# Optimization experiments

Measured on AMD Instinct MI355X. Metric: run time of the kernel, lower is better.

Reference implementation:

```python
import jax, jax.numpy as jnp
import numpy as np

DELTA_VAR = 0.5
DELTA_DIST = 1.5
ALPHA = 1.0
BETA = 1.0
GAMMA = 0.001
IGNORE = 0
C = 20  # static label count: max(target)+1 with labels drawn from [0, 20)


def setup_inputs() -> dict:
    key = jax.random.key(0)
    k1, k2 = jax.random.split(key)
    emb = jax.random.normal(k1, (4, 16, 400, 800), dtype=jnp.float32)
    target = jax.random.randint(k2, (4, 400, 800), 0, 20, dtype=jnp.int32)
    return {"emb": emb, "target": target}


def _safe_norm(sq):
    # L2 norm from squared distance with zero-safe sqrt (matches torch.norm fwd,
    # and gives finite grads at 0 like torch's subgradient convention)
    nz = sq > 0
    return jnp.sqrt(jnp.where(nz, sq, 1.0)) * nz.astype(sq.dtype)


def _loss_one(x, lab):
    # x: (E, H, W), lab: (H, W) int labels in [0, C)
    E = x.shape[0]
    xf = x.reshape(E, -1).T          # (P, E)
    lf = lab.reshape(-1)             # (P,)
    dt = xf.dtype

    counts = jax.ops.segment_sum(jnp.ones_like(lf, dtype=dt), lf, num_segments=C)  # (C,)
    sums = jax.ops.segment_sum(xf, lf, num_segments=C)                              # (C, E)
    means = sums / counts[:, None]                                                  # (C, E)

    keep = jnp.array([c for c in range(C) if c != IGNORE])  # static
    Ck = C - 1
    means_k = means[keep]            # (Ck, E)
    counts_k = counts[keep]          # (Ck,)

    # --- variance (pull) term: distance of each pixel to its own cluster mean ---
    mean_px = means[lf]                                   # (P, E) gather
    d = _safe_norm(jnp.sum((xf - mean_px) ** 2, axis=1))  # (P,)
    mask = (lf != IGNORE).astype(dt)
    hinge = mask * jnp.maximum(d - DELTA_VAR, 0.0) ** 2
    var_per_inst = jax.ops.segment_sum(hinge, lf, num_segments=C)[keep] / counts_k
    variance_term = jnp.sum(var_per_inst) / Ck

    # --- distance (push) term: pairwise hinge between kept cluster means ---
    diff = means_k[:, None, :] - means_k[None, :, :]      # (Ck, Ck, E)
    dm = _safe_norm(jnp.sum(diff ** 2, axis=-1))          # (Ck, Ck)
    repulsion = 2.0 * DELTA_DIST * (1.0 - jnp.eye(Ck, dtype=dt))
    hinged = jnp.maximum(repulsion - dm, 0.0) ** 2
    distance_term = jnp.sum(hinged) / (Ck * (Ck - 1))

    # --- regularizer: mean norm of cluster means ---
    reg_term = jnp.sum(_safe_norm(jnp.sum(means_k ** 2, axis=1))) / Ck

    return ALPHA * variance_term + BETA * distance_term + GAMMA * reg_term


def reference(emb, target):
    losses = jax.vmap(_loss_one)(emb, target)  # (N,)
    return (jnp.sum(losses) / emb.shape[0])[None]  # shape (1,) like torch
```

## Files before the change

kernel.cpp:

```cpp
#include <hip/hip_runtime.h>

#define N_IMG 4
#define E_DIM 16
#define G_PIX 80000
#define C_CLS 20
#define CK 19
#define NREP 8
#define EG 4
#define NEG (E_DIM / EG)
#define SL1 64
#define R1 (G_PIX / SL1)
#define GRID1 (SL1 * NEG * N_IMG)
#define SL2 256
#define R2 ((G_PIX + SL2 - 1) / SL2)
#define GRID2 (SL2 * N_IMG)
#define MSTRIDE 17
#define LS_SLOT 5
#define SCALE_F 16777216.0f
#define INV_SCALE (1.0f / 16777216.0f)

#define SUMS_OFF 0
#define CNT_OFF (N_IMG * C_CLS * E_DIM)
#define LOSS_OFF (CNT_OFF + N_IMG * C_CLS)
#define WS_FLOATS (LOSS_OFF + 1)

static_assert(G_PIX % SL1 == 0, "k_sums slicing must be exact");

__global__ __launch_bounds__(256, 4) void k_sums(const float* __restrict__ emb,
                                                 const int* __restrict__ target,
                                                 float* __restrict__ ws) {
    __shared__ unsigned long long ls[C_CLS][NREP][LS_SLOT];
    __shared__ unsigned int lc[C_CLS][NREP];

    const int tid = threadIdx.x;
    const int b = blockIdx.x;
    const int n = b & 3;
    const int eg = (b >> 2) & (NEG - 1);
    const int slice = b >> 4;
    const int e0 = eg * EG;

    unsigned long long* lsf = &ls[0][0][0];
    for (int i = tid; i < C_CLS * NREP * LS_SLOT; i += 256) lsf[i] = 0ull;
    for (int i = tid; i < C_CLS * NREP; i += 256) (&lc[0][0])[i] = 0u;
    __syncthreads();

    const float4* emb0 = (const float4*)emb + ((size_t)(n * E_DIM + e0)) * G_PIX;
    const int4* tgt4 = (const int4*)target + (size_t)n * G_PIX;
    const int r = tid & (NREP - 1);

#define QADD(p, idx, val) \
    atomicAdd((p) + (idx), (unsigned long long)(long long)__float2int_rn((val) * SCALE_F))

    const int g1 = (slice + 1) * R1;
    for (int g = slice * R1 + tid; g < g1; g += 256) {
        const int4 lb = tgt4[g];
        const float4 v0 = emb0[g];
        const float4 v1 = emb0[G_PIX + g];
        const float4 v2 = emb0[2 * G_PIX + g];
        const float4 v3 = emb0[3 * G_PIX + g];

        unsigned long long* px = &ls[lb.x][r][0];
        unsigned long long* py = &ls[lb.y][r][0];
        unsigned long long* pz = &ls[lb.z][r][0];
        unsigned long long* pw = &ls[lb.w][r][0];
        QADD(px, 0, v0.x); QADD(px, 1, v1.x); QADD(px, 2, v2.x); QADD(px, 3, v3.x);
        QADD(py, 0, v0.y); QADD(py, 1, v1.y); QADD(py, 2, v2.y); QADD(py, 3, v3.y);
        QADD(pz, 0, v0.z); QADD(pz, 1, v1.z); QADD(pz, 2, v2.z); QADD(pz, 3, v3.z);
        QADD(pw, 0, v0.w); QADD(pw, 1, v1.w); QADD(pw, 2, v2.w); QADD(pw, 3, v3.w);
        if (eg == 0) {
            atomicAdd(&lc[lb.x][r], 1u); atomicAdd(&lc[lb.y][r], 1u);
            atomicAdd(&lc[lb.z][r], 1u); atomicAdd(&lc[lb.w][r], 1u);
        }
    }
#undef QADD
    __syncthreads();

    for (int i = tid; i < C_CLS * EG; i += 256) {
        const int c = i >> 2, e1 = i & 3;
        long long q = 0;
#pragma unroll
        for (int rr = 0; rr < NREP; rr++) q += (long long)ls[c][rr][e1];
        atomicAdd(ws + SUMS_OFF + (n * C_CLS + c) * E_DIM + e0 + e1, (float)q * INV_SCALE);
    }
    if (eg == 0) {
        for (int c = tid; c < C_CLS; c += 256) {
            unsigned int s = 0;
#pragma unroll
            for (int rr = 0; rr < NREP; rr++) s += lc[c][rr];
            atomicAdd(ws + CNT_OFF + n * C_CLS + c, (float)s);
        }
    }
}

__global__ __launch_bounds__(256, 4) void k_var(const float* __restrict__ emb,
                                                const int* __restrict__ target,
                                                float* __restrict__ ws) {
    __shared__ float lmean[C_CLS * MSTRIDE];
    __shared__ float lw[C_CLS];
    __shared__ float red[256];

    const int tid = threadIdx.x;
    const int b = blockIdx.x;
    const int n = b & 3;
    const int s2 = b >> 2;

    const float* gsum = ws + SUMS_OFF + n * C_CLS * E_DIM;
    const float* gcnt = ws + CNT_OFF + n * C_CLS;

    for (int i = tid; i < C_CLS * E_DIM; i += 256) {
        const int c = i >> 4, e = i & 15;
        const float cnt = gcnt[c];
        lmean[c * MSTRIDE + e] = (cnt > 0.f) ? gsum[i] / cnt : 0.f;
    }
    if (tid < C_CLS) {
        const float cnt = gcnt[tid];
        lw[tid] = (tid != 0 && cnt > 0.f) ? 1.0f / (cnt * (float)CK) : 0.f;
    }
    __syncthreads();

    float acc = 0.f;
    if (b < N_IMG) {
        for (int idx = tid; idx < CK * CK; idx += 256) {
            const int i = idx / CK + 1, j = idx % CK + 1;
            if (i != j) {
                float sq = 0.f;
#pragma unroll
                for (int e = 0; e < E_DIM; e++) {
                    const float d = lmean[i * MSTRIDE + e] - lmean[j * MSTRIDE + e];
                    sq += d * d;
                }
                const float dm = sqrtf(sq);
                const float h = fmaxf(3.0f - dm, 0.f);
                acc += h * h;
            }
        }
        acc *= 1.0f / (float)(CK * (CK - 1));
        float racc = 0.f;
        for (int c = tid + 1; c < C_CLS; c += 256) {
            float sq = 0.f;
#pragma unroll
            for (int e = 0; e < E_DIM; e++) {
                const float m = lmean[c * MSTRIDE + e];
                sq += m * m;
            }
            racc += sqrtf(sq);
        }
        acc += 0.001f * racc / (float)CK;
    }

    const float4* emb4 = (const float4*)emb + (size_t)n * E_DIM * G_PIX;
    const int4* tgt4 = (const int4*)target + (size_t)n * G_PIX;
    const int gend0 = (s2 + 1) * R2;
    const int gend = (gend0 < G_PIX) ? gend0 : G_PIX;
    for (int g = s2 * R2 + tid; g < gend; g += 256) {
        const int4 lb = tgt4[g];
        const int bx = lb.x * MSTRIDE, by = lb.y * MSTRIDE;
        const int bz = lb.z * MSTRIDE, bw = lb.w * MSTRIDE;
        float sx = 0.f, sy = 0.f, sz = 0.f, sw = 0.f;
#pragma unroll
        for (int e = 0; e < E_DIM; e++) {
            const float4 v = emb4[(size_t)e * G_PIX + g];
            float d;
            d = v.x - lmean[bx + e]; sx += d * d;
            d = v.y - lmean[by + e]; sy += d * d;
            d = v.z - lmean[bz + e]; sz += d * d;
            d = v.w - lmean[bw + e]; sw += d * d;
        }
        float h;
        h = fmaxf(sqrtf(sx) - 0.5f, 0.f); acc += h * h * lw[lb.x];
        h = fmaxf(sqrtf(sy) - 0.5f, 0.f); acc += h * h * lw[lb.y];
        h = fmaxf(sqrtf(sz) - 0.5f, 0.f); acc += h * h * lw[lb.z];
        h = fmaxf(sqrtf(sw) - 0.5f, 0.f); acc += h * h * lw[lb.w];
    }

    red[tid] = acc;
    __syncthreads();
    for (int s = 128; s > 0; s >>= 1) {
        if (tid < s) red[tid] += red[tid + s];
        __syncthreads();
    }
    if (tid == 0) atomicAdd(ws + LOSS_OFF, red[0]);
}

__global__ void k_fin(const float* __restrict__ ws, float* __restrict__ out) {
    out[0] = ws[LOSS_OFF] * 0.25f;
}

extern "C" void kernel_launch(void* const* d_in, const int* in_sizes, int n_in,
                              void* d_out, int out_size, void* d_ws, size_t ws_size,
                              hipStream_t stream) {
    const float* emb = (const float*)d_in[0];
    const int* target = (const int*)d_in[1];
    float* out = (float*)d_out;
    float* ws = (float*)d_ws;

    hipMemsetAsync(d_ws, 0, WS_FLOATS * sizeof(float), stream);
    k_sums<<<dim3(GRID1), 256, 0, stream>>>(emb, target, ws);
    k_var<<<dim3(GRID2), 256, 0, stream>>>(emb, target, ws);
    k_fin<<<1, 1, 0, stream>>>(ws, out);
}
```

Measured before the change: 153.1 us.

## Widen sums embedding groups, batch k_var loads, fold final kernel into last block

k_sums now has each block process 8 embedding channels instead of 4, with twice as many pixel slices, so each block reads the label vector half as often. k_var now loads all 16 embedding float4 values into registers before computing distances, to increase memory-level parallelism. The separate finalize kernel is removed: the last k_var block, found through an atomic counter, writes the scaled loss. Risks include higher register pressure from the 16 float4 registers and the 8-wide group, more LDS per block for the larger slot array, and correctness depending on the atomic ordering in the last-block pattern.

```diff
diff --git a/kernel.cpp b/kernel.cpp
--- a/kernel.cpp
+++ b/kernel.cpp
@@ -6,23 +6,24 @@
 #define C_CLS 20
 #define CK 19
 #define NREP 8
-#define EG 4
+#define EG 8
 #define NEG (E_DIM / EG)
-#define SL1 64
+#define SL1 128
 #define R1 (G_PIX / SL1)
 #define GRID1 (SL1 * NEG * N_IMG)
 #define SL2 256
 #define R2 ((G_PIX + SL2 - 1) / SL2)
 #define GRID2 (SL2 * N_IMG)
 #define MSTRIDE 17
-#define LS_SLOT 5
+#define LS_SLOT 9
 #define SCALE_F 16777216.0f
 #define INV_SCALE (1.0f / 16777216.0f)
 
 #define SUMS_OFF 0
 #define CNT_OFF (N_IMG * C_CLS * E_DIM)
 #define LOSS_OFF (CNT_OFF + N_IMG * C_CLS)
-#define WS_FLOATS (LOSS_OFF + 1)
+#define DONE_OFF (LOSS_OFF + 1)
+#define WS_FLOATS (DONE_OFF + 1)
 
 static_assert(G_PIX % SL1 == 0, "k_sums slicing must be exact");
 
@@ -36,7 +37,7 @@
     const int b = blockIdx.x;
     const int n = b & 3;
     const int eg = (b >> 2) & (NEG - 1);
-    const int slice = b >> 4;
+    const int slice = b >> 3;
     const int e0 = eg * EG;
 
     unsigned long long* lsf = &ls[0][0][0];
@@ -54,19 +55,21 @@
     const int g1 = (slice + 1) * R1;
     for (int g = slice * R1 + tid; g < g1; g += 256) {
         const int4 lb = tgt4[g];
-        const float4 v0 = emb0[g];
-        const float4 v1 = emb0[G_PIX + g];
-        const float4 v2 = emb0[2 * G_PIX + g];
-        const float4 v3 = emb0[3 * G_PIX + g];
+        float4 v[EG];
+#pragma unroll
+        for (int k = 0; k < EG; k++) v[k] = emb0[(size_t)k * G_PIX + g];
 
         unsigned long long* px = &ls[lb.x][r][0];
         unsigned long long* py = &ls[lb.y][r][0];
         unsigned long long* pz = &ls[lb.z][r][0];
         unsigned long long* pw = &ls[lb.w][r][0];
-        QADD(px, 0, v0.x); QADD(px, 1, v1.x); QADD(px, 2, v2.x); QADD(px, 3, v3.x);
-        QADD(py, 0, v0.y); QADD(py, 1, v1.y); QADD(py, 2, v2.y); QADD(py, 3, v3.y);
-        QADD(pz, 0, v0.z); QADD(pz, 1, v1.z); QADD(pz, 2, v2.z); QADD(pz, 3, v3.z);
-        QADD(pw, 0, v0.w); QADD(pw, 1, v1.w); QADD(pw, 2, v2.w); QADD(pw, 3, v3.w);
+#pragma unroll
+        for (int k = 0; k < EG; k++) {
+            QADD(px, k, v[k].x);
+            QADD(py, k, v[k].y);
+            QADD(pz, k, v[k].z);
+            QADD(pw, k, v[k].w);
+        }
         if (eg == 0) {
             atomicAdd(&lc[lb.x][r], 1u); atomicAdd(&lc[lb.y][r], 1u);
             atomicAdd(&lc[lb.z][r], 1u); atomicAdd(&lc[lb.w][r], 1u);
@@ -76,7 +79,7 @@
     __syncthreads();
 
     for (int i = tid; i < C_CLS * EG; i += 256) {
-        const int c = i >> 2, e1 = i & 3;
+        const int c = i >> 3, e1 = i & 7;
         long long q = 0;
 #pragma unroll
         for (int rr = 0; rr < NREP; rr++) q += (long long)ls[c][rr][e1];
@@ -94,7 +97,8 @@
 
 __global__ __launch_bounds__(256, 4) void k_var(const float* __restrict__ emb,
                                                 const int* __restrict__ target,
-                                                float* __restrict__ ws) {
+                                                float* __restrict__ ws,
+                                                float* __restrict__ out) {
     __shared__ float lmean[C_CLS * MSTRIDE];
     __shared__ float lw[C_CLS];
     __shared__ float red[256];
@@ -154,17 +158,20 @@
     const int gend = (gend0 < G_PIX) ? gend0 : G_PIX;
     for (int g = s2 * R2 + tid; g < gend; g += 256) {
         const int4 lb = tgt4[g];
+        float4 v[E_DIM];
+#pragma unroll
+        for (int e = 0; e < E_DIM; e++) v[e] = emb4[(size_t)e * G_PIX + g];
+
         const int bx = lb.x * MSTRIDE, by = lb.y * MSTRIDE;
         const int bz = lb.z * MSTRIDE, bw = lb.w * MSTRIDE;
         float sx = 0.f, sy = 0.f, sz = 0.f, sw = 0.f;
 #pragma unroll
         for (int e = 0; e < E_DIM; e++) {
-            const float4 v = emb4[(size_t)e * G_PIX + g];
             float d;
-            d = v.x - lmean[bx + e]; sx += d * d;
-            d = v.y - lmean[by + e]; sy += d * d;
-            d = v.z - lmean[bz + e]; sz += d * d;
-            d = v.w - lmean[bw + e]; sw += d * d;
+            d = v[e].x - lmean[bx + e]; sx += d * d;
+            d = v[e].y - lmean[by + e]; sy += d * d;
+            d = v[e].z - lmean[bz + e]; sz += d * d;
+            d = v[e].w - lmean[bw + e]; sw += d * d;
         }
         float h;
         h = fmaxf(sqrtf(sx) - 0.5f, 0.f); acc += h * h * lw[lb.x];
@@ -179,11 +186,18 @@
         if (tid < s) red[tid] += red[tid + s];
         __syncthreads();
     }
-    if (tid == 0) atomicAdd(ws + LOSS_OFF, red[0]);
-}
-
-__global__ void k_fin(const float* __restrict__ ws, float* __restrict__ out) {
-    out[0] = ws[LOSS_OFF] * 0.25f;
+    if (tid == 0) {
+        atomicAdd(ws + LOSS_OFF, red[0]);
+        __threadfence();
+        unsigned* done = (unsigned*)(ws + DONE_OFF);
+        const unsigned arr = __hip_atomic_fetch_add(done, 1u, __ATOMIC_ACQ_REL,
+                                                    __HIP_MEMORY_SCOPE_AGENT);
+        if (arr == GRID2 - 1) {
+            const float l = __hip_atomic_load(ws + LOSS_OFF, __ATOMIC_RELAXED,
+                                              __HIP_MEMORY_SCOPE_AGENT);
+            out[0] = l * 0.25f;
+        }
+    }
 }
 
 extern "C" void kernel_launch(void* const* d_in, const int* in_sizes, int n_in,
@@ -196,6 +210,5 @@
 
     hipMemsetAsync(d_ws, 0, WS_FLOATS * sizeof(float), stream);
     k_sums<<<dim3(GRID1), 256, 0, stream>>>(emb, target, ws);
-    k_var<<<dim3(GRID2), 256, 0, stream>>>(emb, target, ws);
-    k_fin<<<1, 1, 0, stream>>>(ws, out);
+    k_var<<<dim3(GRID2), 256, 0, stream>>>(emb, target, ws, out);
 }
```

Result: slower. 174.3 us (+13.8%).
